# Kernel tuning notes

Hardware: AMD Instinct MI355X
Metric: run time of the kernel (lower is better)

The kernel has to match this reference:

```python
import jax, jax.numpy as jnp
import numpy as np

B, N, E, H = 2, 4096, 768, 8
D = E // H
SCALING = float(D ** 0.5)


def setup_inputs() -> dict:
    key = jax.random.key(0)
    ks = jax.random.split(key, 9)
    s = 1.0 / np.sqrt(E)
    return {
        "x": jax.random.normal(ks[0], (B, N, E), dtype=jnp.float32),
        "Wq": jax.random.normal(ks[1], (E, E), dtype=jnp.float32) * s,
        "bq": jax.random.normal(ks[2], (E,), dtype=jnp.float32) * s,
        "Wk": jax.random.normal(ks[3], (E, E), dtype=jnp.float32) * s,
        "bk": jax.random.normal(ks[4], (E,), dtype=jnp.float32) * s,
        "Wv": jax.random.normal(ks[5], (E, E), dtype=jnp.float32) * s,
        "bv": jax.random.normal(ks[6], (E,), dtype=jnp.float32) * s,
        "Wo": jax.random.normal(ks[7], (E, E), dtype=jnp.float32) * s,
        "bo": jax.random.normal(ks[8], (E,), dtype=jnp.float32) * s,
    }


def reference(x, Wq, bq, Wk, bk, Wv, bv, Wo, bo):
    b, n, e = x.shape
    # projections, split heads: [b, n, e] -> [b, h, n, d]
    def split_heads(y):
        return y.reshape(b, n, H, D).transpose(0, 2, 1, 3)
    q = split_heads(x @ Wq + bq)
    k = split_heads(x @ Wk + bk)
    v = split_heads(x @ Wv + bv)
    # full quadratic attention matrix, as in the original einsum
    energy = jnp.einsum("bhqd,bhkd->bhqk", q, k)  # [b, h, n, n]
    # NOTE: original divides by scaling AFTER softmax (not before)
    att = jax.nn.softmax(energy, axis=-1) / SCALING
    out = jnp.einsum("bhqk,bhkd->bhqd", att, v)  # [b, h, n, d]
    out = out.transpose(0, 2, 1, 3).reshape(b, n, e)  # merge heads
    return out @ Wo + bo
```

## Files before the change

kernel.cpp:

```cpp
#include <hip/hip_runtime.h>
#include <hip/hip_bf16.h>


typedef unsigned short u16;
typedef unsigned long long u64;
typedef __attribute__((ext_vector_type(4))) float f32x4;
typedef __attribute__((ext_vector_type(8))) _Float16 h16x8;
typedef __attribute__((ext_vector_type(8))) u16 u16x8;

#define DEVI static __device__ __forceinline__

#define GLD16(gp, lp)                                                          \
  __builtin_amdgcn_global_load_lds(                                            \
      (const __attribute__((address_space(1))) void*)(gp),                     \
      (__attribute__((address_space(3))) void*)(lp), 16, 0, 0)

DEVI u16 f2h(float f) {
  _Float16 h = (_Float16)f;
  return __builtin_bit_cast(u16, h);
}

DEVI f32x4 mfma16(u16x8 a, u16x8 b, f32x4 c) {
  return __builtin_amdgcn_mfma_f32_16x16x32_f16(
      __builtin_bit_cast(h16x8, a), __builtin_bit_cast(h16x8, b), c, 0, 0, 0);
}

__global__ void k_cast(const float* __restrict__ x, u16* __restrict__ xh, int n8) {
  int i = blockIdx.x * blockDim.x + threadIdx.x;
  if (i >= n8) return;
  const f32x4* p = (const f32x4*)x + (size_t)i * 2;
  f32x4 a = p[0], b = p[1];
  u16x8 o;
  #pragma unroll
  for (int u = 0; u < 4; ++u) { o[u] = f2h(a[u]); o[4 + u] = f2h(b[u]); }
  *((u16x8*)xh + i) = o;
}

__global__ void k_wt(const float* __restrict__ Wq, const float* __restrict__ Wk,
                     const float* __restrict__ Wv, const float* __restrict__ Wo,
                     u16* __restrict__ wT) {
  __shared__ __align__(16) float T[64 * 68];
  int bid = blockIdx.x;
  int mat = bid / 144, tt = bid % 144;
  int tr = tt / 12, tc = tt % 12;
  const float* W = (mat == 0) ? Wq : (mat == 1) ? Wk : (mat == 2) ? Wv : Wo;
  int k0 = tr * 64, n0 = tc * 64;
  int t = threadIdx.x;
  #pragma unroll
  for (int ii = 0; ii < 4; ++ii) {
    int i = t + 256 * ii, r = i >> 4, c4 = i & 15;
    f32x4 v = *(const f32x4*)(W + (size_t)(k0 + r) * 768 + n0 + c4 * 4);
    *(f32x4*)(&T[r * 68 + c4 * 4]) = v;
  }
  __syncthreads();
  #pragma unroll
  for (int ii = 0; ii < 2; ++ii) {
    int i = t + 256 * ii, nn = i & 63, kc8 = i >> 6;
    u16x8 o;
    #pragma unroll
    for (int u = 0; u < 8; ++u) o[u] = f2h(T[(kc8 * 8 + u) * 68 + nn]);
    *(u16x8*)(wT + (size_t)mat * 589824 + (size_t)(n0 + nn) * 768 + k0 + kc8 * 8) = o;
  }
}

__global__ void k_vt(const u16* __restrict__ V, u16* __restrict__ Vt) {
  __shared__ __align__(16) u16 L[64 * 104];
  int bid = blockIdx.x, bh = bid >> 6, nb = bid & 63;
  int n0 = nb * 64, t = threadIdx.x;
  const u16* src = V + ((size_t)bh * 4096 + n0) * 96;
  #pragma unroll
  for (int ii = 0; ii < 3; ++ii) {
    int i = t + 256 * ii, r = i / 12, c8 = i % 12;
    *(u16x8*)(&L[r * 104 + c8 * 8]) = *(const u16x8*)(src + (size_t)i * 8);
  }
  __syncthreads();
  #pragma unroll
  for (int jj = 0; jj < 3; ++jj) {
    int d = (t & 31) + 32 * jj, c8 = t >> 5;
    u16x8 o;
    #pragma unroll
    for (int u = 0; u < 8; ++u) o[u] = L[(c8 * 8 + u) * 104 + d];
    *(u16x8*)(Vt + ((size_t)bh * 96 + d) * 4096 + n0 + c8 * 8) = o;
  }
}

template <int MODE>
__global__ __launch_bounds__(256) void k_gemm(
    const u16* __restrict__ A, const u16* __restrict__ BT,
    const float* __restrict__ bias0, const float* __restrict__ bias1,
    const float* __restrict__ bias2,
    u16* __restrict__ Qb, u16* __restrict__ Kb, u16* __restrict__ Vb,
    float* __restrict__ Out) {
  __shared__ __align__(16) u16 Alds[128 * 32];
  __shared__ __align__(16) u16 Blds[128 * 32];
  const int m0 = blockIdx.x * 128, n0 = blockIdx.y * 128;
  const int t = threadIdx.x, w = t >> 6, lane = t & 63;
  const int g = lane >> 4, c = lane & 15;
  const int wr = w >> 1, wc = w & 1;

  f32x4 acc[4][4] = {};

  for (int k0 = 0; k0 < 768; k0 += 32) {
    __syncthreads();
    #pragma unroll
    for (int ii = 0; ii < 2; ++ii) {
      int i = t + 256 * ii;
      int lbase = (i & ~63) * 8;
      GLD16(A + (size_t)(m0 + (i >> 2)) * 768 + k0 + (i & 3) * 8, &Alds[lbase]);
      GLD16(BT + (size_t)(n0 + (i >> 2)) * 768 + k0 + (i & 3) * 8, &Blds[lbase]);
    }
    __syncthreads();
    u16x8 af[4], bf[4];
    #pragma unroll
    for (int mt = 0; mt < 4; ++mt)
      af[mt] = *(u16x8*)(&Alds[(wr * 64 + mt * 16 + c) * 32 + g * 8]);
    #pragma unroll
    for (int nt = 0; nt < 4; ++nt)
      bf[nt] = *(u16x8*)(&Blds[(wc * 64 + nt * 16 + c) * 32 + g * 8]);
    #pragma unroll
    for (int mt = 0; mt < 4; ++mt)
      #pragma unroll
      for (int nt = 0; nt < 4; ++nt)
        acc[mt][nt] = mfma16(af[mt], bf[nt], acc[mt][nt]);
  }

  if (MODE == 0) {
    const int mat = n0 / 768;
    const float* bias = (mat == 0) ? bias0 : (mat == 1) ? bias1 : bias2;
    u16* dst = (mat == 0) ? Qb : (mat == 1) ? Kb : Vb;
    const int nbase = n0 - mat * 768;
    #pragma unroll
    for (int mt = 0; mt < 4; ++mt)
      #pragma unroll
      for (int nt = 0; nt < 4; ++nt) {
        int ncol = nbase + wc * 64 + nt * 16 + c;
        int h = ncol / 96, d = ncol % 96;
        float bi = bias[ncol];
        #pragma unroll
        for (int r = 0; r < 4; ++r) {
          int mrow = m0 + wr * 64 + mt * 16 + g * 4 + r;
          int b = mrow >> 12, ntok = mrow & 4095;
          dst[((size_t)((b * 8 + h) * 4096 + ntok)) * 96 + d] =
              f2h(acc[mt][nt][r] + bi);
        }
      }
  } else {
    #pragma unroll
    for (int mt = 0; mt < 4; ++mt)
      #pragma unroll
      for (int nt = 0; nt < 4; ++nt) {
        int ncol = n0 + wc * 64 + nt * 16 + c;
        float bi = bias0[ncol];
        #pragma unroll
        for (int r = 0; r < 4; ++r) {
          int mrow = m0 + wr * 64 + mt * 16 + g * 4 + r;
          Out[(size_t)mrow * 768 + ncol] = acc[mt][nt][r] + bi;
        }
      }
  }
}

__global__ __launch_bounds__(256) void k_attn(
    const u16* __restrict__ Q, const u16* __restrict__ K,
    const u16* __restrict__ Vt, u16* __restrict__ attn) {
  __shared__ __align__(16) u16 smem[23040];
  u16* Klds  = smem;
  u16* Vtlds = smem + 6656;
  u16* Plds  = smem + 12800;

  const int bid = blockIdx.x;
  const int bh = bid >> 5, qb = bid & 31;
  const int t = threadIdx.x, w = t >> 6, lane = t & 63;
  const int g = lane >> 4, c = lane & 15;
  const int q0 = qb * 128;

  u16x8 qf[3][2];
  #pragma unroll
  for (int qc = 0; qc < 2; ++qc) {
    const size_t qoff = ((size_t)bh * 4096 + q0 + w * 32 + qc * 16 + c) * 96;
    #pragma unroll
    for (int kc = 0; kc < 3; ++kc)
      qf[kc][qc] = *(const u16x8*)(Q + qoff + kc * 32 + g * 8);
  }

  f32x4 acc_o[6][2] = {};
  float m[2] = {-1e30f, -1e30f}, s[2] = {0.f, 0.f};

  const u16* Kbb = K + (size_t)bh * 4096 * 96;
  const u16* Vtb = Vt + (size_t)bh * 96 * 4096;

  #pragma unroll 1
  for (int kv0 = 0; kv0 < 4096; kv0 += 64) {
    __syncthreads();
    #pragma unroll
    for (int ii = 0; ii < 4; ++ii) {
      int i = t + 256 * ii;
      if (i < 832) {
        int row = i / 13, c8 = i % 13;
        int c8s = (c8 < 12) ? c8 : 0;
        GLD16(Kbb + (size_t)(kv0 + row) * 96 + c8s * 8, &Klds[(i & ~63) * 8]);
      }
    }
    #pragma unroll
    for (int ii = 0; ii < 3; ++ii) {
      int i = t + 256 * ii, d = i >> 3, c8 = i & 7;
      GLD16(Vtb + (size_t)d * 4096 + kv0 + ((c8 ^ (d & 7)) * 8), &Vtlds[(i & ~63) * 8]);
    }
    __syncthreads();

    f32x4 et[4][2] = {};
    #pragma unroll
    for (int kc = 0; kc < 3; ++kc)
      #pragma unroll
      for (int mt = 0; mt < 4; ++mt) {
        u16x8 kf = *(u16x8*)(&Klds[(mt * 16 + c) * 104 + kc * 32 + g * 8]);
        #pragma unroll
        for (int qc = 0; qc < 2; ++qc)
          et[mt][qc] = mfma16(kf, qf[kc][qc], et[mt][qc]);
      }

    #pragma unroll
    for (int qc = 0; qc < 2; ++qc) {
      float tmax = -1e30f;
      #pragma unroll
      for (int mt = 0; mt < 4; ++mt)
        #pragma unroll
        for (int r = 0; r < 4; ++r) tmax = fmaxf(tmax, et[mt][qc][r]);
      tmax = fmaxf(tmax, __shfl_xor(tmax, 16));
      tmax = fmaxf(tmax, __shfl_xor(tmax, 32));
      float mnew = fmaxf(m[qc], tmax);
      float scale = __expf(m[qc] - mnew);
      float psum = 0.f;
      #pragma unroll
      for (int mt = 0; mt < 4; ++mt)
        #pragma unroll
        for (int r = 0; r < 4; ++r) {
          float p = __expf(et[mt][qc][r] - mnew);
          et[mt][qc][r] = p; psum += p;
        }
      psum += __shfl_xor(psum, 16);
      psum += __shfl_xor(psum, 32);
      s[qc] = s[qc] * scale + psum;
      m[qc] = mnew;
      #pragma unroll
      for (int dt = 0; dt < 6; ++dt)
        #pragma unroll
        for (int r = 0; r < 4; ++r) acc_o[dt][qc][r] *= scale;

      u16* P = Plds + (w * 2 + qc) * 1280;
      #pragma unroll
      for (int mt = 0; mt < 4; ++mt) {
        unsigned p0 = (unsigned)f2h(et[mt][qc][0]) |
                      ((unsigned)f2h(et[mt][qc][1]) << 16);
        unsigned p1 = (unsigned)f2h(et[mt][qc][2]) |
                      ((unsigned)f2h(et[mt][qc][3]) << 16);
        *(u64*)(&P[c * 80 + mt * 16 + g * 4]) = (u64)p0 | ((u64)p1 << 32);
      }
    }
    u16x8 pf[2][2];
    #pragma unroll
    for (int qc = 0; qc < 2; ++qc)
      #pragma unroll
      for (int kb = 0; kb < 2; ++kb)
        pf[qc][kb] = *(u16x8*)(&Plds[(w * 2 + qc) * 1280 + c * 80 + kb * 32 + g * 8]);
    #pragma unroll
    for (int dt = 0; dt < 6; ++dt)
      #pragma unroll
      for (int kb = 0; kb < 2; ++kb) {
        u16x8 vf = *(u16x8*)(&Vtlds[(dt * 16 + c) * 64 +
                                    (((kb * 4 + g) ^ (c & 7)) * 8)]);
        #pragma unroll
        for (int qc = 0; qc < 2; ++qc)
          acc_o[dt][qc] = mfma16(vf, pf[qc][kb], acc_o[dt][qc]);
      }
  }

  __syncthreads();
  u16* O = smem;
  #pragma unroll
  for (int qc = 0; qc < 2; ++qc) {
    const float inv = 1.0f / (s[qc] * 9.797958971132712f);
    #pragma unroll
    for (int dt = 0; dt < 6; ++dt)
      #pragma unroll
      for (int rp = 0; rp < 2; ++rp) {
        unsigned pk = (unsigned)f2h(acc_o[dt][qc][2 * rp] * inv) |
                      ((unsigned)f2h(acc_o[dt][qc][2 * rp + 1] * inv) << 16);
        *(unsigned*)(&O[(w * 32 + qc * 16 + c) * 96 + dt * 16 + g * 4 + 2 * rp]) = pk;
      }
  }
  __syncthreads();
  const int b = bh >> 3, h = bh & 7;
  #pragma unroll
  for (int ii = 0; ii < 6; ++ii) {
    int i = t + 256 * ii, r = i / 12, c8 = i % 12;
    u16x8 v = *(u16x8*)(&O[r * 96 + c8 * 8]);
    *(u16x8*)(attn + ((size_t)(b * 4096 + q0 + r)) * 768 + h * 96 + c8 * 8) = v;
  }
}

extern "C" void kernel_launch(void* const* d_in, const int* in_sizes, int n_in,
                              void* d_out, int out_size, void* d_ws, size_t ws_size,
                              hipStream_t stream) {
  const float* x  = (const float*)d_in[0];
  const float* Wq = (const float*)d_in[1];
  const float* bq = (const float*)d_in[2];
  const float* Wk = (const float*)d_in[3];
  const float* bk = (const float*)d_in[4];
  const float* Wv = (const float*)d_in[5];
  const float* bv = (const float*)d_in[6];
  const float* Wo = (const float*)d_in[7];
  const float* bo = (const float*)d_in[8];
  float* out = (float*)d_out;

  char* ws = (char*)d_ws;
  size_t off = 0;
  auto alloc = [&](size_t bytes) {
    void* p = ws + off;
    off += (bytes + 1023) & ~(size_t)1023;
    return p;
  };
  const size_t SZ = (size_t)16 * 4096 * 96 * 2;
  u16* xh    = (u16*)alloc((size_t)8192 * 768 * 2);
  u16* wT    = (u16*)alloc((size_t)4 * 768 * 768 * 2);
  u16* Qb    = (u16*)alloc(SZ);
  u16* Kb    = (u16*)alloc(SZ);
  u16* Vb    = (u16*)alloc(SZ);
  u16* Vtb   = (u16*)alloc(SZ);
  u16* attnb = (u16*)alloc(SZ);
  (void)ws_size; (void)in_sizes; (void)n_in; (void)out_size;

  k_cast<<<3072, 256, 0, stream>>>(x, xh, 786432);
  k_wt<<<576, 256, 0, stream>>>(Wq, Wk, Wv, Wo, wT);
  k_gemm<0><<<dim3(64, 18), 256, 0, stream>>>(xh, wT, bq, bk, bv,
                                              Qb, Kb, Vb, nullptr);
  k_vt<<<1024, 256, 0, stream>>>(Vb, Vtb);
  k_attn<<<512, 256, 0, stream>>>(Qb, Kb, Vtb, attnb);
  k_gemm<1><<<dim3(64, 6), 256, 0, stream>>>(attnb, wT + (size_t)3 * 589824,
                                             bo, nullptr, nullptr,
                                             nullptr, nullptr, nullptr, out);
}
```

Measured before the change: 334.2 us.

## Double-buffer GEMM and attention loads, use exp2 softmax with lazy rescaling

```diff
diff --git a/kernel.cpp b/kernel.cpp
--- a/kernel.cpp
+++ b/kernel.cpp
@@ -6,6 +6,7 @@
 typedef unsigned long long u64;
 typedef __attribute__((ext_vector_type(4))) float f32x4;
 typedef __attribute__((ext_vector_type(8))) _Float16 h16x8;
+typedef __attribute__((ext_vector_type(2))) __fp16 fp16x2;
 typedef __attribute__((ext_vector_type(8))) u16 u16x8;
 
 #define DEVI static __device__ __forceinline__
@@ -14,10 +15,27 @@
   __builtin_amdgcn_global_load_lds(                                            \
       (const __attribute__((address_space(1))) void*)(gp),                     \
       (__attribute__((address_space(3))) void*)(lp), 16, 0, 0)
+#define VM_WAIT6() asm volatile("s_waitcnt vmcnt(6)" ::: "memory")
+#define VM_WAIT4() asm volatile("s_waitcnt vmcnt(4)" ::: "memory")
+#define VM_WAIT0() asm volatile("s_waitcnt vmcnt(0)" ::: "memory")
+#define BARRAW()   asm volatile("s_barrier" ::: "memory")
 
 DEVI u16 f2h(float f) {
   _Float16 h = (_Float16)f;
   return __builtin_bit_cast(u16, h);
+}
+
+DEVI unsigned pkrtz(float a, float b) {
+  fp16x2 h = __builtin_amdgcn_cvt_pkrtz(a, b);
+  return __builtin_bit_cast(unsigned, h);
+}
+
+DEVI float exp2fast(float x) {
+#if __has_builtin(__builtin_amdgcn_exp2f)
+  return __builtin_amdgcn_exp2f(x);
+#else
+  return __expf(x * 0.6931471805599453f);
+#endif
 }
 
 DEVI f32x4 mfma16(u16x8 a, u16x8 b, f32x4 c) {
@@ -91,43 +109,56 @@
     const float* __restrict__ bias2,
     u16* __restrict__ Qb, u16* __restrict__ Kb, u16* __restrict__ Vb,
     float* __restrict__ Out) {
-  __shared__ __align__(16) u16 Alds[128 * 32];
-  __shared__ __align__(16) u16 Blds[128 * 32];
+  __shared__ __align__(16) u16 sg[16384];
   const int m0 = blockIdx.x * 128, n0 = blockIdx.y * 128;
   const int t = threadIdx.x, w = t >> 6, lane = t & 63;
   const int g = lane >> 4, c = lane & 15;
   const int wr = w >> 1, wc = w & 1;
 
+  const u16* ap[2]; const u16* bp[2]; int lo[2];
+  #pragma unroll
+  for (int ii = 0; ii < 2; ++ii) {
+    int i = t + 256 * ii;
+    ap[ii] = A + (size_t)(m0 + (i >> 2)) * 768 + (i & 3) * 8;
+    bp[ii] = BT + (size_t)(n0 + (i >> 2)) * 768 + (i & 3) * 8;
+    lo[ii] = (i & ~63) * 8;
+  }
+  auto STAGE = [&](int buf) {
+    #pragma unroll
+    for (int ii = 0; ii < 2; ++ii) {
+      GLD16(ap[ii], &sg[buf * 4096 + lo[ii]]);
+      GLD16(bp[ii], &sg[8192 + buf * 4096 + lo[ii]]);
+      ap[ii] += 32; bp[ii] += 32;
+    }
+  };
+
   f32x4 acc[4][4] = {};
-
-  for (int k0 = 0; k0 < 768; k0 += 32) {
-    __syncthreads();
-    #pragma unroll
-    for (int ii = 0; ii < 2; ++ii) {
-      int i = t + 256 * ii;
-      int lbase = (i & ~63) * 8;
-      GLD16(A + (size_t)(m0 + (i >> 2)) * 768 + k0 + (i & 3) * 8, &Alds[lbase]);
-      GLD16(BT + (size_t)(n0 + (i >> 2)) * 768 + k0 + (i & 3) * 8, &Blds[lbase]);
-    }
-    __syncthreads();
+  STAGE(0);
+  #pragma unroll 1
+  for (int kk = 0; kk < 24; ++kk) {
+    const int cur = kk & 1;
+    if (kk < 23) { STAGE(cur ^ 1); VM_WAIT4(); } else { VM_WAIT0(); }
+    BARRAW();
     u16x8 af[4], bf[4];
     #pragma unroll
     for (int mt = 0; mt < 4; ++mt)
-      af[mt] = *(u16x8*)(&Alds[(wr * 64 + mt * 16 + c) * 32 + g * 8]);
+      af[mt] = *(u16x8*)(&sg[cur * 4096 + (wr * 64 + mt * 16 + c) * 32 + g * 8]);
     #pragma unroll
     for (int nt = 0; nt < 4; ++nt)
-      bf[nt] = *(u16x8*)(&Blds[(wc * 64 + nt * 16 + c) * 32 + g * 8]);
+      bf[nt] = *(u16x8*)(&sg[8192 + cur * 4096 + (wc * 64 + nt * 16 + c) * 32 + g * 8]);
     #pragma unroll
     for (int mt = 0; mt < 4; ++mt)
       #pragma unroll
       for (int nt = 0; nt < 4; ++nt)
         acc[mt][nt] = mfma16(af[mt], bf[nt], acc[mt][nt]);
+    BARRAW();
   }
 
   if (MODE == 0) {
     const int mat = n0 / 768;
     const float* bias = (mat == 0) ? bias0 : (mat == 1) ? bias1 : bias2;
     u16* dst = (mat == 0) ? Qb : (mat == 1) ? Kb : Vb;
+    const float qsc = (mat == 0) ? 1.44269504f : 1.0f;
     const int nbase = n0 - mat * 768;
     #pragma unroll
     for (int mt = 0; mt < 4; ++mt)
@@ -141,7 +172,7 @@
           int mrow = m0 + wr * 64 + mt * 16 + g * 4 + r;
           int b = mrow >> 12, ntok = mrow & 4095;
           dst[((size_t)((b * 8 + h) * 4096 + ntok)) * 96 + d] =
-              f2h(acc[mt][nt][r] + bi);
+              f2h((acc[mt][nt][r] + bi) * qsc);
         }
       }
   } else {
@@ -163,10 +194,7 @@
 __global__ __launch_bounds__(256) void k_attn(
     const u16* __restrict__ Q, const u16* __restrict__ K,
     const u16* __restrict__ Vt, u16* __restrict__ attn) {
-  __shared__ __align__(16) u16 smem[23040];
-  u16* Klds  = smem;
-  u16* Vtlds = smem + 6656;
-  u16* Plds  = smem + 12800;
+  __shared__ __align__(16) u16 smem[34816];
 
   const int bid = blockIdx.x;
   const int bh = bid >> 5, qb = bid & 31;
@@ -182,78 +210,94 @@
     for (int kc = 0; kc < 3; ++kc)
       qf[kc][qc] = *(const u16x8*)(Q + qoff + kc * 32 + g * 8);
   }
+  VM_WAIT0();
+
+  const u16* Kbb = K + (size_t)bh * 4096 * 96;
+  const u16* Vtb = Vt + (size_t)bh * 96 * 4096;
+  const u16* ks[3]; const u16* vs[3]; int ko[3], vo[3];
+  #pragma unroll
+  for (int ii = 0; ii < 3; ++ii) {
+    int ci = t + 256 * ii;
+    ks[ii] = Kbb + ci * 8;
+    int d = ci >> 3, c8 = ci & 7;
+    vs[ii] = Vtb + (size_t)d * 4096 + ((c8 ^ (d & 7)) * 8);
+    ko[ii] = (ci & ~63) * 8;
+    vo[ii] = 12288 + (ci & ~63) * 8;
+  }
+  auto STAGE = [&](int buf) {
+    #pragma unroll
+    for (int ii = 0; ii < 3; ++ii) {
+      GLD16(ks[ii], &smem[buf * 6144 + ko[ii]]);
+      GLD16(vs[ii], &smem[buf * 6144 + vo[ii]]);
+      ks[ii] += 6144;
+      vs[ii] += 64;
+    }
+  };
 
   f32x4 acc_o[6][2] = {};
   float m[2] = {-1e30f, -1e30f}, s[2] = {0.f, 0.f};
-
-  const u16* Kbb = K + (size_t)bh * 4096 * 96;
-  const u16* Vtb = Vt + (size_t)bh * 96 * 4096;
-
+  u16* Pw = &smem[24576 + w * 2560];
+
+  STAGE(0);
   #pragma unroll 1
-  for (int kv0 = 0; kv0 < 4096; kv0 += 64) {
-    __syncthreads();
-    #pragma unroll
-    for (int ii = 0; ii < 4; ++ii) {
-      int i = t + 256 * ii;
-      if (i < 832) {
-        int row = i / 13, c8 = i % 13;
-        int c8s = (c8 < 12) ? c8 : 0;
-        GLD16(Kbb + (size_t)(kv0 + row) * 96 + c8s * 8, &Klds[(i & ~63) * 8]);
-      }
-    }
-    #pragma unroll
-    for (int ii = 0; ii < 3; ++ii) {
-      int i = t + 256 * ii, d = i >> 3, c8 = i & 7;
-      GLD16(Vtb + (size_t)d * 4096 + kv0 + ((c8 ^ (d & 7)) * 8), &Vtlds[(i & ~63) * 8]);
-    }
-    __syncthreads();
+  for (int tt = 0; tt < 64; ++tt) {
+    const int cur = tt & 1;
+    if (tt < 63) { STAGE(cur ^ 1); VM_WAIT6(); } else { VM_WAIT0(); }
+    BARRAW();
+    const u16* Kl = &smem[cur * 6144];
+    const u16* Vl = &smem[12288 + cur * 6144];
 
     f32x4 et[4][2] = {};
     #pragma unroll
     for (int kc = 0; kc < 3; ++kc)
       #pragma unroll
       for (int mt = 0; mt < 4; ++mt) {
-        u16x8 kf = *(u16x8*)(&Klds[(mt * 16 + c) * 104 + kc * 32 + g * 8]);
-        #pragma unroll
-        for (int qc = 0; qc < 2; ++qc)
-          et[mt][qc] = mfma16(kf, qf[kc][qc], et[mt][qc]);
+        u16x8 kf = *(const u16x8*)(&Kl[(mt * 16 + c) * 96 + kc * 32 + g * 8]);
+        et[mt][0] = mfma16(kf, qf[kc][0], et[mt][0]);
+        et[mt][1] = mfma16(kf, qf[kc][1], et[mt][1]);
       }
 
     #pragma unroll
     for (int qc = 0; qc < 2; ++qc) {
-      float tmax = -1e30f;
-      #pragma unroll
-      for (int mt = 0; mt < 4; ++mt)
-        #pragma unroll
-        for (int r = 0; r < 4; ++r) tmax = fmaxf(tmax, et[mt][qc][r]);
+      float t0 = fmaxf(fmaxf(et[0][qc][0], et[0][qc][1]),
+                       fmaxf(et[0][qc][2], et[0][qc][3]));
+      float t1 = fmaxf(fmaxf(et[1][qc][0], et[1][qc][1]),
+                       fmaxf(et[1][qc][2], et[1][qc][3]));
+      float t2 = fmaxf(fmaxf(et[2][qc][0], et[2][qc][1]),
+                       fmaxf(et[2][qc][2], et[2][qc][3]));
+      float t3 = fmaxf(fmaxf(et[3][qc][0], et[3][qc][1]),
+                       fmaxf(et[3][qc][2], et[3][qc][3]));
+      float tmax = fmaxf(fmaxf(t0, t1), fmaxf(t2, t3));
       tmax = fmaxf(tmax, __shfl_xor(tmax, 16));
       tmax = fmaxf(tmax, __shfl_xor(tmax, 32));
-      float mnew = fmaxf(m[qc], tmax);
-      float scale = __expf(m[qc] - mnew);
+      bool upd = tmax > m[qc] + 12.0f;
+      float mnew = upd ? tmax : m[qc];
+      if (__any(upd)) {
+        float sc = exp2fast(m[qc] - mnew);
+        s[qc] *= sc;
+        #pragma unroll
+        for (int dt = 0; dt < 6; ++dt)
+          #pragma unroll
+          for (int r = 0; r < 4; ++r) acc_o[dt][qc][r] *= sc;
+      }
+      m[qc] = mnew;
       float psum = 0.f;
       #pragma unroll
       for (int mt = 0; mt < 4; ++mt)
         #pragma unroll
         for (int r = 0; r < 4; ++r) {
-          float p = __expf(et[mt][qc][r] - mnew);
+          float p = exp2fast(et[mt][qc][r] - mnew);
           et[mt][qc][r] = p; psum += p;
         }
       psum += __shfl_xor(psum, 16);
       psum += __shfl_xor(psum, 32);
-      s[qc] = s[qc] * scale + psum;
-      m[qc] = mnew;
-      #pragma unroll
-      for (int dt = 0; dt < 6; ++dt)
-        #pragma unroll
-        for (int r = 0; r < 4; ++r) acc_o[dt][qc][r] *= scale;
-
-      u16* P = Plds + (w * 2 + qc) * 1280;
+      s[qc] += psum;
+
+      u16* P = Pw + qc * 1280;
       #pragma unroll
       for (int mt = 0; mt < 4; ++mt) {
-        unsigned p0 = (unsigned)f2h(et[mt][qc][0]) |
-                      ((unsigned)f2h(et[mt][qc][1]) << 16);
-        unsigned p1 = (unsigned)f2h(et[mt][qc][2]) |
-                      ((unsigned)f2h(et[mt][qc][3]) << 16);
+        unsigned p0 = pkrtz(et[mt][qc][0], et[mt][qc][1]);
+        unsigned p1 = pkrtz(et[mt][qc][2], et[mt][qc][3]);
         *(u64*)(&P[c * 80 + mt * 16 + g * 4]) = (u64)p0 | ((u64)p1 << 32);
       }
     }
@@ -262,17 +306,16 @@
     for (int qc = 0; qc < 2; ++qc)
       #pragma unroll
       for (int kb = 0; kb < 2; ++kb)
-        pf[qc][kb] = *(u16x8*)(&Plds[(w * 2 + qc) * 1280 + c * 80 + kb * 32 + g * 8]);
+        pf[qc][kb] = *(u16x8*)(&Pw[qc * 1280 + c * 80 + kb * 32 + g * 8]);
     #pragma unroll
     for (int dt = 0; dt < 6; ++dt)
       #pragma unroll
       for (int kb = 0; kb < 2; ++kb) {
-        u16x8 vf = *(u16x8*)(&Vtlds[(dt * 16 + c) * 64 +
-                                    (((kb * 4 + g) ^ (c & 7)) * 8)]);
-        #pragma unroll
-        for (int qc = 0; qc < 2; ++qc)
-          acc_o[dt][qc] = mfma16(vf, pf[qc][kb], acc_o[dt][qc]);
-      }
+        u16x8 vf = *(u16x8*)(&Vl[(dt * 16 + c) * 64 + (((kb * 4 + g) ^ (c & 7)) * 8)]);
+        acc_o[dt][0] = mfma16(vf, pf[0][kb], acc_o[dt][0]);
+        acc_o[dt][1] = mfma16(vf, pf[1][kb], acc_o[dt][1]);
+      }
+    BARRAW();
   }
 
   __syncthreads();
```

Result: faster. 314.3 us (-6.0%).
